# Performance work log

Hardware: AMD Instinct MI355X
Metric: run time of the kernel (lower is better)

## Reference

```python
import jax, jax.numpy as jnp
import numpy as np

B, S, D, H, F = 4, 1024, 1024, 16, 4096
DH = D // H  # 64


def _xavier(key, shape):
    fan_in, fan_out = shape[-2], shape[-1]
    limit = np.sqrt(6.0 / (fan_in + fan_out)).astype(np.float32)
    return jax.random.uniform(key, shape, jnp.float32, -limit, limit)


def setup_inputs() -> dict:
    key = jax.random.key(0)
    ks = jax.random.split(key, 24)
    inp = {
        'decoder_input': jax.random.normal(ks[0], (B, S, D), jnp.float32),
        'encoder_output': jax.random.normal(ks[1], (B, S, D), jnp.float32),
        'mask': jnp.broadcast_to(jnp.tril(jnp.ones((S, S), jnp.bool_)), (B, S, S)),
    }
    # self-attention per-head Q/K/V weights stacked over heads: (H, D, DH)
    for i, p in enumerate(['sa', 'ca']):
        base = 2 + i * 8
        inp[f'{p}_wq'] = _xavier(ks[base + 0], (H, D, DH))
        inp[f'{p}_wk'] = _xavier(ks[base + 1], (H, D, DH))
        inp[f'{p}_wv'] = _xavier(ks[base + 2], (H, D, DH))
        inp[f'{p}_bq'] = jnp.zeros((H, DH), jnp.float32)
        inp[f'{p}_bk'] = jnp.zeros((H, DH), jnp.float32)
        inp[f'{p}_bv'] = jnp.zeros((H, DH), jnp.float32)
        inp[f'{p}_wo'] = _xavier(ks[base + 3], (H * DH, D))
        inp[f'{p}_bo'] = jnp.zeros((D,), jnp.float32)
    inp['ff_w1'] = _xavier(ks[18], (D, F))
    inp['ff_b1'] = jnp.zeros((F,), jnp.float32)
    inp['ff_w2'] = _xavier(ks[19], (F, D))
    inp['ff_b2'] = jnp.zeros((D,), jnp.float32)
    for j in (1, 2, 3):
        inp[f'ln{j}_g'] = jnp.ones((D,), jnp.float32)
        inp[f'ln{j}_b'] = jnp.zeros((D,), jnp.float32)
    return inp


def _layernorm(x, g, b, eps=1e-12):
    # torch x.var() default is unbiased (ddof=1) -- match it
    mean = jnp.mean(x, axis=-1, keepdims=True)
    var = jnp.var(x, axis=-1, keepdims=True, ddof=1)
    return g * (x - mean) * jax.lax.rsqrt(var + eps) + b


def _mha(q_in, k_in, v_in, wq, bq, wk, bk, wv, bv, wo, bo, mask=None):
    scale = np.float32(1.0 / np.sqrt(DH))
    q = jnp.einsum('bsd,hde->bhse', q_in, wq) + bq[None, :, None, :]
    k = jnp.einsum('bsd,hde->bhse', k_in, wk) + bk[None, :, None, :]
    v = jnp.einsum('bsd,hde->bhse', v_in, wv) + bv[None, :, None, :]
    scores = jnp.einsum('bhqe,bhke->bhqk', q, k) * scale
    if mask is not None:
        scores = jnp.where(mask[:, None, :, :], scores, jnp.float32(-1e9))
    attn = jax.nn.softmax(scores, axis=-1)
    out = jnp.einsum('bhqk,bhke->bhqe', attn, v)  # (B,H,S,DH)
    out = out.transpose(0, 2, 1, 3).reshape(q_in.shape[0], q_in.shape[1], H * DH)
    return out @ wo + bo


def reference(decoder_input, encoder_output, mask,
              sa_wq, sa_wk, sa_wv, sa_bq, sa_bk, sa_bv, sa_wo, sa_bo,
              ca_wq, ca_wk, ca_wv, ca_bq, ca_bk, ca_bv, ca_wo, ca_bo,
              ff_w1, ff_b1, ff_w2, ff_b2,
              ln1_g, ln1_b, ln2_g, ln2_b, ln3_g, ln3_b):
    # dropout is identity (eval mode)
    out1 = _mha(decoder_input, decoder_input, decoder_input,
                sa_wq, sa_bq, sa_wk, sa_bk, sa_wv, sa_bv, sa_wo, sa_bo, mask)
    out1 = _layernorm(out1 + decoder_input, ln1_g, ln1_b)
    out2 = _mha(out1, encoder_output, encoder_output,
                ca_wq, ca_bq, ca_wk, ca_bk, ca_wv, ca_bv, ca_wo, ca_bo, None)
    out2 = _layernorm(out2 + out1, ln2_g, ln2_b)
    out3 = jax.nn.relu(out2 @ ff_w1 + ff_b1) @ ff_w2 + ff_b2
    out3 = _layernorm(out3 + out2, ln3_g, ln3_b)
    return out3
```

## Files before the change

kernel.cpp:

```cpp
#include <hip/hip_runtime.h>
#include <hip/hip_bf16.h>

using bf16 = __hip_bfloat16;
typedef __attribute__((ext_vector_type(8))) short bf16x8;
typedef __attribute__((ext_vector_type(4))) float f32x4;

__device__ __forceinline__ float toF(float x) { return x; }
__device__ __forceinline__ float toF(bf16 x) { return __bfloat162float(x); }

template <typename T> __device__ __forceinline__ T fromF(float x);
template <> __device__ __forceinline__ float fromF<float>(float x) { return x; }
template <> __device__ __forceinline__ bf16 fromF<bf16>(float x) { return __float2bfloat16(x); }

__device__ __forceinline__ unsigned short f2bu(float f) {
    bf16 h = __float2bfloat16(f);
    return *reinterpret_cast<unsigned short*>(&h);
}
__device__ __forceinline__ float bu2f(unsigned short u) {
    unsigned int x = ((unsigned int)u) << 16;
    return __uint_as_float(x);
}

__device__ __forceinline__ void gload16(const unsigned short* g, unsigned short* l) {
    __builtin_amdgcn_global_load_lds(
        (const __attribute__((address_space(1))) unsigned int*)g,
        (__attribute__((address_space(3))) unsigned int*)l, 16, 0, 0);
}

__global__ __launch_bounds__(256) void cvt_k(const float* __restrict__ X,
                                             unsigned short* __restrict__ Y, int n)
{
    int i = (blockIdx.x * 256 + threadIdx.x) * 4;
    if (i >= n) return;
    float4 v = *(const float4*)(X + i);
    ushort4 o;
    o.x = f2bu(v.x); o.y = f2bu(v.y); o.z = f2bu(v.z); o.w = f2bu(v.w);
    *(ushort4*)(Y + i) = o;
}

struct WPtrs { const float* w[3]; };

template <bool HEADED>
__global__ __launch_bounds__(256) void wtrans_k(
    WPtrs wp, unsigned short* __restrict__ Wt, int K, int N)
{
    __shared__ float t[32][33];
    const float* __restrict__ W = wp.w[blockIdx.z];
    unsigned short* __restrict__ out = Wt + (size_t)blockIdx.z * K * N;
    const int k0 = blockIdx.x * 32, n0 = blockIdx.y * 32;
    const int tx = threadIdx.x & 31, ty = threadIdx.x >> 5;
#pragma unroll
    for (int i = 0; i < 4; i++) {
        int k = k0 + ty + 8 * i, n = n0 + tx;
        float v;
        if constexpr (HEADED) v = W[((size_t)(n >> 6) * K + k) * 64 + (n & 63)];
        else                  v = W[(size_t)k * N + n];
        t[ty + 8 * i][tx] = v;
    }
    __syncthreads();
#pragma unroll
    for (int i = 0; i < 4; i++)
        out[(size_t)(n0 + ty + 8 * i) * K + k0 + tx] = f2bu(t[tx][ty + 8 * i]);
}

template <typename TO, typename TR, bool RELU, bool HASRES, int BN>
__global__ __launch_bounds__(256) void gemm_mfma(
    const unsigned short* __restrict__ A, const unsigned short* __restrict__ Bt,
    const float* __restrict__ bias, const TR* __restrict__ res,
    TO* __restrict__ C, int M, int N, int K)
{
    constexpr int MI = (BN == 128) ? 4 : 2;
    __shared__ __align__(16) unsigned short As[128 * 64];
    __shared__ __align__(16) unsigned short Bs[BN * 64];

    const int tid = threadIdx.x;
    const int lane = tid & 63, wv = tid >> 6;
    const int quad = lane >> 4, col = lane & 15;
    const int m0 = blockIdx.y * 128, n0 = blockIdx.x * BN;
    const int wm = (BN == 128) ? (wv >> 1) * 64 : wv * 32;
    const int wn = (BN == 128) ? (wv & 1) * 64 : 0;

    f32x4 acc[MI][4];
#pragma unroll
    for (int i = 0; i < MI; i++)
#pragma unroll
        for (int j = 0; j < 4; j++) acc[i][j] = (f32x4){0.f, 0.f, 0.f, 0.f};

    const int rowl = (wv << 3) + (lane >> 3);
    const int xq = (lane & 7) ^ (lane >> 3);
    const unsigned short* Ag = A + (size_t)(m0 + rowl) * K + xq * 8;
    const unsigned short* Bg = Bt + (size_t)(n0 + rowl) * K + xq * 8;
    unsigned short* AsW = As + wv * 512;
    unsigned short* BsW = Bs + wv * 512;

    const int xr = col & 7;

    for (int k0 = 0; k0 < K; k0 += 64) {
        __syncthreads();
#pragma unroll
        for (int r = 0; r < 4; r++)
            gload16(Ag + (size_t)(r * 32) * K + k0, AsW + r * 2048);
#pragma unroll
        for (int r = 0; r < BN / 32; r++)
            gload16(Bg + (size_t)(r * 32) * K + k0, BsW + r * 2048);
        __syncthreads();

#pragma unroll
        for (int kk = 0; kk < 2; kk++) {
            const int cq = ((kk << 2) + quad) ^ xr;
            bf16x8 af[MI], bfr[4];
#pragma unroll
            for (int mi = 0; mi < MI; mi++)
                af[mi] = *(const bf16x8*)(As + (wm + mi * 16 + col) * 64 + cq * 8);
#pragma unroll
            for (int ni = 0; ni < 4; ni++)
                bfr[ni] = *(const bf16x8*)(Bs + (wn + ni * 16 + col) * 64 + cq * 8);
#pragma unroll
            for (int mi = 0; mi < MI; mi++)
#pragma unroll
                for (int ni = 0; ni < 4; ni++)
                    acc[mi][ni] = __builtin_amdgcn_mfma_f32_16x16x32_bf16(
                        af[mi], bfr[ni], acc[mi][ni], 0, 0, 0);
        }
    }

    float bv[4];
#pragma unroll
    for (int ni = 0; ni < 4; ni++) bv[ni] = bias[n0 + wn + ni * 16 + col];
#pragma unroll
    for (int mi = 0; mi < MI; mi++) {
#pragma unroll
        for (int r = 0; r < 4; r++) {
            int m = m0 + wm + mi * 16 + quad * 4 + r;
#pragma unroll
            for (int ni = 0; ni < 4; ni++) {
                int n = n0 + wn + ni * 16 + col;
                float v = acc[mi][ni][r] + bv[ni];
                if constexpr (HASRES) v += toF(res[(size_t)m * N + n]);
                if constexpr (RELU) v = v > 0.f ? v : 0.f;
                C[(size_t)m * N + n] = fromF<TO>(v);
            }
        }
    }
}

struct SegArgs {
    const float* bias[3];
    unsigned short* out[3];
};

__global__ __launch_bounds__(256) void gemm_seg(
    const unsigned short* __restrict__ A, const unsigned short* __restrict__ Bt,
    SegArgs sp, int M, int K, int transSeg)
{
    __shared__ __align__(16) unsigned short As[128 * 64];
    __shared__ __align__(16) unsigned short Bs[128 * 64];

    const int tid = threadIdx.x;
    const int lane = tid & 63, wv = tid >> 6;
    const int quad = lane >> 4, col = lane & 15;
    const int m0 = blockIdx.y * 128, n0 = blockIdx.x * 128;
    const int wm = (wv >> 1) * 64, wn = (wv & 1) * 64;

    f32x4 acc[4][4];
#pragma unroll
    for (int i = 0; i < 4; i++)
#pragma unroll
        for (int j = 0; j < 4; j++) acc[i][j] = (f32x4){0.f, 0.f, 0.f, 0.f};

    const int rowl = (wv << 3) + (lane >> 3);
    const int xq = (lane & 7) ^ (lane >> 3);
    const unsigned short* Ag = A + (size_t)(m0 + rowl) * K + xq * 8;
    const unsigned short* Bg = Bt + (size_t)(n0 + rowl) * K + xq * 8;
    unsigned short* AsW = As + wv * 512;
    unsigned short* BsW = Bs + wv * 512;
    const int xr = col & 7;

    for (int k0 = 0; k0 < K; k0 += 64) {
        __syncthreads();
#pragma unroll
        for (int r = 0; r < 4; r++)
            gload16(Ag + (size_t)(r * 32) * K + k0, AsW + r * 2048);
#pragma unroll
        for (int r = 0; r < 4; r++)
            gload16(Bg + (size_t)(r * 32) * K + k0, BsW + r * 2048);
        __syncthreads();

#pragma unroll
        for (int kk = 0; kk < 2; kk++) {
            const int cq = ((kk << 2) + quad) ^ xr;
            bf16x8 af[4], bfr[4];
#pragma unroll
            for (int mi = 0; mi < 4; mi++)
                af[mi] = *(const bf16x8*)(As + (wm + mi * 16 + col) * 64 + cq * 8);
#pragma unroll
            for (int ni = 0; ni < 4; ni++)
                bfr[ni] = *(const bf16x8*)(Bs + (wn + ni * 16 + col) * 64 + cq * 8);
#pragma unroll
            for (int mi = 0; mi < 4; mi++)
#pragma unroll
                for (int ni = 0; ni < 4; ni++)
                    acc[mi][ni] = __builtin_amdgcn_mfma_f32_16x16x32_bf16(
                        af[mi], bfr[ni], acc[mi][ni], 0, 0, 0);
        }
    }

    const int seg = n0 >> 10;
    const float* bias = sp.bias[seg];
    unsigned short* out = sp.out[seg];
    const int nb = (n0 & 1023) + wn;
    const bool trans = (seg == transSeg);

    float bv[4];
#pragma unroll
    for (int ni = 0; ni < 4; ni++) bv[ni] = bias[nb + ni * 16 + col];
#pragma unroll
    for (int mi = 0; mi < 4; mi++) {
#pragma unroll
        for (int r = 0; r < 4; r++) {
            int m = m0 + wm + mi * 16 + quad * 4 + r;
#pragma unroll
            for (int ni = 0; ni < 4; ni++) {
                int nl = nb + ni * 16 + col;
                float v = acc[mi][ni][r] + bv[ni];
                if (trans)
                    out[((size_t)(m >> 10) * 1024 + nl) * 1024 + (m & 1023)] = f2bu(v);
                else
                    out[(size_t)m * 1024 + nl] = f2bu(v);
            }
        }
    }
}

template <bool CAUSAL>
__global__ __launch_bounds__(256) void fattn_k(
    const unsigned short* __restrict__ Q, const unsigned short* __restrict__ K,
    const unsigned short* __restrict__ Vt, unsigned short* __restrict__ O, int S)
{
    const int qt = CAUSAL ? ((int)gridDim.x - 1 - (int)blockIdx.x) : blockIdx.x;
    const int h = blockIdx.y, b = blockIdx.z;
    const int H64 = 1024;
    const int tid = threadIdx.x;
    const int w = tid >> 6, lane = tid & 63;
    const int quad = lane >> 4, col = lane & 15;

    __shared__ __align__(16) unsigned short Ks[64 * 72];
    __shared__ __align__(16) unsigned short Vs[64 * 72];
    __shared__ __align__(16) unsigned short Ps[4 * 16 * 72];

    const int qBase = qt * 64 + w * 16;
    const size_t qrow = ((size_t)b * S + qBase + col) * H64 + h * 64;

    const float qscale = 0.125f * 1.44269504f;
    bf16x8 qf0, qf1;
    {
        bf16x8 r0 = *(const bf16x8*)(Q + qrow + quad * 8);
        bf16x8 r1 = *(const bf16x8*)(Q + qrow + quad * 8 + 32);
#pragma unroll
        for (int j = 0; j < 8; j++) {
            qf0[j] = (short)f2bu(bu2f((unsigned short)r0[j]) * qscale);
            qf1[j] = (short)f2bu(bu2f((unsigned short)r1[j]) * qscale);
        }
    }

    f32x4 o[4];
#pragma unroll
    for (int g = 0; g < 4; g++) o[g] = (f32x4){0.f, 0.f, 0.f, 0.f};
    float m_run[4], l_run[4];
#pragma unroll
    for (int r = 0; r < 4; r++) { m_run[r] = -1e30f; l_run[r] = 0.f; }

    const int skey = tid >> 2;
    const int sseg = (tid & 3) * 16;
    const size_t kgbase = (size_t)b * S * H64 + h * 64;
    const size_t vgbase = ((size_t)b * 1024 + h * 64) * (size_t)S;

    const int nkt = CAUSAL ? (qt + 1) : (S >> 6);
    unsigned short* Pw = Ps + w * (16 * 72);

    for (int kt = 0; kt < nkt; kt++) {
        __syncthreads();
        {
            const unsigned short* kg_ = K + kgbase + (size_t)(kt * 64 + skey) * H64;
            const unsigned short* vg_ = Vt + vgbase + (size_t)skey * S + kt * 64;
            *(uint4*)(Ks + skey * 72 + sseg)     = *(const uint4*)(kg_ + sseg);
            *(uint4*)(Ks + skey * 72 + sseg + 8) = *(const uint4*)(kg_ + sseg + 8);
            *(uint4*)(Vs + skey * 72 + sseg)     = *(const uint4*)(vg_ + sseg);
            *(uint4*)(Vs + skey * 72 + sseg + 8) = *(const uint4*)(vg_ + sseg + 8);
        }
        __syncthreads();

        f32x4 s[4];
#pragma unroll
        for (int kg = 0; kg < 4; kg++) {
            bf16x8 k0 = *(const bf16x8*)(Ks + (kg * 16 + col) * 72 + quad * 8);
            bf16x8 k1 = *(const bf16x8*)(Ks + (kg * 16 + col) * 72 + quad * 8 + 32);
            f32x4 a = (f32x4){0.f, 0.f, 0.f, 0.f};
            a = __builtin_amdgcn_mfma_f32_16x16x32_bf16(qf0, k0, a, 0, 0, 0);
            a = __builtin_amdgcn_mfma_f32_16x16x32_bf16(qf1, k1, a, 0, 0, 0);
            s[kg] = a;
        }

        if (CAUSAL && kt == qt) {
#pragma unroll
            for (int kg = 0; kg < 4; kg++)
#pragma unroll
                for (int r = 0; r < 4; r++) {
                    int key = kg * 16 + col;
                    int q = w * 16 + quad * 4 + r;
                    if (key > q) s[kg][r] = -1e30f;
                }
        }

        float mx[4];
#pragma unroll
        for (int r = 0; r < 4; r++) {
            float m2 = fmaxf(fmaxf(s[0][r], s[1][r]), fmaxf(s[2][r], s[3][r]));
#pragma unroll
            for (int off = 1; off < 16; off <<= 1)
                m2 = fmaxf(m2, __shfl_xor(m2, off));
            mx[r] = m2;
        }

        bool defer = (mx[0] <= m_run[0] + 8.f) & (mx[1] <= m_run[1] + 8.f)
                   & (mx[2] <= m_run[2] + 8.f) & (mx[3] <= m_run[3] + 8.f);
        if (!__all(defer)) {
#pragma unroll
            for (int r = 0; r < 4; r++) {
                float mnew = fmaxf(m_run[r], mx[r]);
                float alpha = exp2f(m_run[r] - mnew);
                l_run[r] *= alpha;
#pragma unroll
                for (int g = 0; g < 4; g++) o[g][r] *= alpha;
                m_run[r] = mnew;
            }
        }

#pragma unroll
        for (int r = 0; r < 4; r++) {
            float ps = 0.f;
#pragma unroll
            for (int kg = 0; kg < 4; kg++) {
                float e = exp2f(s[kg][r] - m_run[r]);
                s[kg][r] = e;
                ps += e;
            }
#pragma unroll
            for (int off = 1; off < 16; off <<= 1)
                ps += __shfl_xor(ps, off);
            l_run[r] += ps;
        }

#pragma unroll
        for (int kg = 0; kg < 4; kg++)
#pragma unroll
            for (int r = 0; r < 4; r++)
                Pw[(quad * 4 + r) * 72 + kg * 16 + col] = f2bu(s[kg][r]);
        __syncthreads();

        bf16x8 p0 = *(const bf16x8*)(Pw + col * 72 + quad * 8);
        bf16x8 p1 = *(const bf16x8*)(Pw + col * 72 + quad * 8 + 32);

#pragma unroll
        for (int g = 0; g < 4; g++) {
            bf16x8 v0 = *(const bf16x8*)(Vs + (g * 16 + col) * 72 + quad * 8);
            bf16x8 v1 = *(const bf16x8*)(Vs + (g * 16 + col) * 72 + quad * 8 + 32);
            o[g] = __builtin_amdgcn_mfma_f32_16x16x32_bf16(p0, v0, o[g], 0, 0, 0);
            o[g] = __builtin_amdgcn_mfma_f32_16x16x32_bf16(p1, v1, o[g], 0, 0, 0);
        }
    }

    const size_t orow = ((size_t)b * S + qBase) * H64 + h * 64;
#pragma unroll
    for (int r = 0; r < 4; r++) {
        float inv = 1.f / l_run[r];
        int q = quad * 4 + r;
#pragma unroll
        for (int g = 0; g < 4; g++)
            O[orow + (size_t)q * H64 + g * 16 + col] = f2bu(o[g][r] * inv);
    }
}

template <typename TO>
__global__ __launch_bounds__(256) void ln_k(
    const float* __restrict__ X, const float* __restrict__ g,
    const float* __restrict__ bb, TO* __restrict__ O, int D)
{
    const int row = blockIdx.x;
    const int tid = threadIdx.x;
    __shared__ float xs[1024];
    __shared__ float red[256];
    const float* x = X + (size_t)row * D;

    float s = 0.f;
    for (int i = tid; i < D; i += 256) { float v = x[i]; xs[i] = v; s += v; }
    red[tid] = s;
    __syncthreads();
    for (int t = 128; t > 0; t >>= 1) {
        if (tid < t) red[tid] += red[tid + t];
        __syncthreads();
    }
    const float mean = red[0] / (float)D;
    __syncthreads();

    float s2 = 0.f;
    for (int i = tid; i < D; i += 256) { float d = xs[i] - mean; s2 += d * d; }
    red[tid] = s2;
    __syncthreads();
    for (int t = 128; t > 0; t >>= 1) {
        if (tid < t) red[tid] += red[tid + t];
        __syncthreads();
    }
    const float rstd = rsqrtf(red[0] / (float)(D - 1) + 1e-12f);

    TO* o = O + (size_t)row * D;
    for (int i = tid; i < D; i += 256)
        o[i] = fromF<TO>(g[i] * (xs[i] - mean) * rstd + bb[i]);
}

extern "C" void kernel_launch(void* const* d_in, const int* in_sizes, int n_in,
                              void* d_out, int out_size, void* d_ws, size_t ws_size,
                              hipStream_t stream)
{
    const int Bb = 4, S = 1024, D = 1024, F = 4096;
    const int M = Bb * S;
    const int H = 16;

    const float* dec = (const float*)d_in[0];
    const float* enc = (const float*)d_in[1];

    int base = 2;
    if (n_in >= 29 && in_sizes[2] == Bb * S * S) base = 3;

    const float* sa_wq = (const float*)d_in[base + 0];
    const float* sa_wk = (const float*)d_in[base + 1];
    const float* sa_wv = (const float*)d_in[base + 2];
    const float* sa_bq = (const float*)d_in[base + 3];
    const float* sa_bk = (const float*)d_in[base + 4];
    const float* sa_bv = (const float*)d_in[base + 5];
    const float* sa_wo = (const float*)d_in[base + 6];
    const float* sa_bo = (const float*)d_in[base + 7];
    const float* ca_wq = (const float*)d_in[base + 8];
    const float* ca_wk = (const float*)d_in[base + 9];
    const float* ca_wv = (const float*)d_in[base + 10];
    const float* ca_bq = (const float*)d_in[base + 11];
    const float* ca_bk = (const float*)d_in[base + 12];
    const float* ca_bv = (const float*)d_in[base + 13];
    const float* ca_wo = (const float*)d_in[base + 14];
    const float* ca_bo = (const float*)d_in[base + 15];
    const float* ff_w1 = (const float*)d_in[base + 16];
    const float* ff_b1 = (const float*)d_in[base + 17];
    const float* ff_w2 = (const float*)d_in[base + 18];
    const float* ff_b2 = (const float*)d_in[base + 19];
    const float* ln1_g = (const float*)d_in[base + 20];
    const float* ln1_b = (const float*)d_in[base + 21];
    const float* ln2_g = (const float*)d_in[base + 22];
    const float* ln2_b = (const float*)d_in[base + 23];
    const float* ln3_g = (const float*)d_in[base + 24];
    const float* ln3_b = (const float*)d_in[base + 25];

    const size_t E = (size_t)M * D;
    const size_t M1 = (size_t)1024 * 1024;
    float* SUM = (float*)d_ws;
    bf16* O1 = (bf16*)(SUM + E);
    bf16* O2 = O1 + E;
    bf16* Q  = O2 + E;
    bf16* Kb = Q + E;
    bf16* Vt = Kb + E;
    bf16* AO = Vt + E;
    bf16* HID = Q;
    unsigned short* decB = (unsigned short*)AO;
    unsigned short* Wt   = (unsigned short*)d_out;
    unsigned short* encB = (unsigned short*)d_out + 4 * 1024 * 1024;

    dim3 blk(256);
    dim3 gQKV(3 * D / 128, M / 128);
    dim3 gKV(2 * D / 128, M / 128);
    dim3 gN(D / 64, M / 128);
    dim3 gF(F / 128, M / 128);
    dim3 gA(S / 64, H, Bb);
    dim3 gT3(D / 32, D / 32, 3);
    dim3 gT2z(D / 32, D / 32, 2);
    dim3 gT(D / 32, D / 32, 1);
    dim3 gT1(D / 32, F / 32, 1);
    dim3 gT2(F / 32, D / 32, 1);

    cvt_k<<<M * D / 1024, blk, 0, stream>>>(dec, decB, M * D);
    cvt_k<<<M * D / 1024, blk, 0, stream>>>(enc, encB, M * D);

    {
        WPtrs wp; wp.w[0] = sa_wq; wp.w[1] = sa_wk; wp.w[2] = sa_wv;
        wtrans_k<true><<<gT3, blk, 0, stream>>>(wp, Wt, D, D);
    }
    {
        SegArgs sp;
        sp.bias[0] = sa_bq; sp.bias[1] = sa_bk; sp.bias[2] = sa_bv;
        sp.out[0] = (unsigned short*)Q; sp.out[1] = (unsigned short*)Kb;
        sp.out[2] = (unsigned short*)Vt;
        gemm_seg<<<gQKV, blk, 0, stream>>>(decB, Wt, sp, M, D, 2);
    }
    fattn_k<true><<<gA, blk, 0, stream>>>((const unsigned short*)Q, (const unsigned short*)Kb,
                                          (const unsigned short*)Vt, (unsigned short*)AO, S);
    {
        WPtrs wp; wp.w[0] = sa_wo; wp.w[1] = nullptr; wp.w[2] = nullptr;
        wtrans_k<false><<<gT, blk, 0, stream>>>(wp, Wt, D, D);
    }
    gemm_mfma<float, float, false, true, 64><<<gN, blk, 0, stream>>>(
        (const unsigned short*)AO, Wt, sa_bo, dec, SUM, M, D, D);
    ln_k<bf16><<<M, blk, 0, stream>>>(SUM, ln1_g, ln1_b, O1, D);

    {
        WPtrs wp; wp.w[0] = ca_wq; wp.w[1] = nullptr; wp.w[2] = nullptr;
        wtrans_k<true><<<gT, blk, 0, stream>>>(wp, Wt, D, D);
    }
    gemm_mfma<bf16, float, false, false, 64><<<gN, blk, 0, stream>>>(
        (const unsigned short*)O1, Wt, ca_bq, (const float*)nullptr, Q, M, D, D);
    {
        WPtrs wp; wp.w[0] = ca_wk; wp.w[1] = ca_wv; wp.w[2] = nullptr;
        wtrans_k<true><<<gT2z, blk, 0, stream>>>(wp, Wt, D, D);
    }
    {
        SegArgs sp;
        sp.bias[0] = ca_bk; sp.bias[1] = ca_bv; sp.bias[2] = nullptr;
        sp.out[0] = (unsigned short*)Kb; sp.out[1] = (unsigned short*)Vt;
        sp.out[2] = nullptr;
        gemm_seg<<<gKV, blk, 0, stream>>>(encB, Wt, sp, M, D, 1);
    }
    fattn_k<false><<<gA, blk, 0, stream>>>((const unsigned short*)Q, (const unsigned short*)Kb,
                                           (const unsigned short*)Vt, (unsigned short*)AO, S);
    {
        WPtrs wp; wp.w[0] = ca_wo; wp.w[1] = nullptr; wp.w[2] = nullptr;
        wtrans_k<false><<<gT, blk, 0, stream>>>(wp, Wt, D, D);
    }
    gemm_mfma<float, bf16, false, true, 64><<<gN, blk, 0, stream>>>(
        (const unsigned short*)AO, Wt, ca_bo, O1, SUM, M, D, D);
    ln_k<bf16><<<M, blk, 0, stream>>>(SUM, ln2_g, ln2_b, O2, D);

    {
        WPtrs wp; wp.w[0] = ff_w1; wp.w[1] = nullptr; wp.w[2] = nullptr;
        wtrans_k<false><<<gT1, blk, 0, stream>>>(wp, Wt, D, F);
    }
    gemm_mfma<bf16, float, true, false, 128><<<gF, blk, 0, stream>>>(
        (const unsigned short*)O2, Wt, ff_b1, (const float*)nullptr, HID, M, F, D);
    {
        WPtrs wp; wp.w[0] = ff_w2; wp.w[1] = nullptr; wp.w[2] = nullptr;
        wtrans_k<false><<<gT2, blk, 0, stream>>>(wp, Wt, F, D);
    }
    gemm_mfma<float, bf16, false, true, 64><<<gN, blk, 0, stream>>>(
        (const unsigned short*)HID, Wt, ff_b2, O2, SUM, M, D, F);
    ln_k<float><<<M, blk, 0, stream>>>(SUM, ln3_g, ln3_b, (float*)d_out, D);
}
```

Before: 600.8 us.

## Load K/V fragments directly from global in flash attention, use fast exp2

The flash-attention kernel no longer stages K and V tiles through shared memory. Each wave now reads its MFMA operand fragments straight from global memory, which removes the per-tile shared-memory copy and all block-wide barriers, including the one after the per-wave P write. The exp2f calls become the hardware exp2 builtin. In exchange, the four waves of a block each fetch the same K/V data, relying on caches, and global-load latency is exposed with no software prefetch. The P store and reload now rely on in-order LDS access within a wave rather than an explicit barrier.

```diff
diff --git a/kernel.cpp b/kernel.cpp
--- a/kernel.cpp
+++ b/kernel.cpp
@@ -19,6 +19,14 @@
 __device__ __forceinline__ float bu2f(unsigned short u) {
     unsigned int x = ((unsigned int)u) << 16;
     return __uint_as_float(x);
+}
+
+__device__ __forceinline__ float fexp2(float x) {
+#if __has_builtin(__builtin_amdgcn_exp2f)
+    return __builtin_amdgcn_exp2f(x);
+#else
+    return __expf(x * 0.69314718f);
+#endif
 }
 
 __device__ __forceinline__ void gload16(const unsigned short* g, unsigned short* l) {
@@ -244,8 +252,6 @@
     const int w = tid >> 6, lane = tid & 63;
     const int quad = lane >> 4, col = lane & 15;
 
-    __shared__ __align__(16) unsigned short Ks[64 * 72];
-    __shared__ __align__(16) unsigned short Vs[64 * 72];
     __shared__ __align__(16) unsigned short Ps[4 * 16 * 72];
 
     const int qBase = qt * 64 + w * 16;
@@ -270,8 +276,6 @@
 #pragma unroll
     for (int r = 0; r < 4; r++) { m_run[r] = -1e30f; l_run[r] = 0.f; }
 
-    const int skey = tid >> 2;
-    const int sseg = (tid & 3) * 16;
     const size_t kgbase = (size_t)b * S * H64 + h * 64;
     const size_t vgbase = ((size_t)b * 1024 + h * 64) * (size_t)S;
 
@@ -279,22 +283,13 @@
     unsigned short* Pw = Ps + w * (16 * 72);
 
     for (int kt = 0; kt < nkt; kt++) {
-        __syncthreads();
-        {
-            const unsigned short* kg_ = K + kgbase + (size_t)(kt * 64 + skey) * H64;
-            const unsigned short* vg_ = Vt + vgbase + (size_t)skey * S + kt * 64;
-            *(uint4*)(Ks + skey * 72 + sseg)     = *(const uint4*)(kg_ + sseg);
-            *(uint4*)(Ks + skey * 72 + sseg + 8) = *(const uint4*)(kg_ + sseg + 8);
-            *(uint4*)(Vs + skey * 72 + sseg)     = *(const uint4*)(vg_ + sseg);
-            *(uint4*)(Vs + skey * 72 + sseg + 8) = *(const uint4*)(vg_ + sseg + 8);
-        }
-        __syncthreads();
-
         f32x4 s[4];
 #pragma unroll
         for (int kg = 0; kg < 4; kg++) {
-            bf16x8 k0 = *(const bf16x8*)(Ks + (kg * 16 + col) * 72 + quad * 8);
-            bf16x8 k1 = *(const bf16x8*)(Ks + (kg * 16 + col) * 72 + quad * 8 + 32);
+            const unsigned short* kr =
+                K + kgbase + (size_t)(kt * 64 + kg * 16 + col) * H64 + quad * 8;
+            bf16x8 k0 = *(const bf16x8*)(kr);
+            bf16x8 k1 = *(const bf16x8*)(kr + 32);
             f32x4 a = (f32x4){0.f, 0.f, 0.f, 0.f};
             a = __builtin_amdgcn_mfma_f32_16x16x32_bf16(qf0, k0, a, 0, 0, 0);
             a = __builtin_amdgcn_mfma_f32_16x16x32_bf16(qf1, k1, a, 0, 0, 0);
@@ -328,7 +323,7 @@
 #pragma unroll
             for (int r = 0; r < 4; r++) {
                 float mnew = fmaxf(m_run[r], mx[r]);
-                float alpha = exp2f(m_run[r] - mnew);
+                float alpha = fexp2(m_run[r] - mnew);
                 l_run[r] *= alpha;
 #pragma unroll
                 for (int g = 0; g < 4; g++) o[g][r] *= alpha;
@@ -341,7 +336,7 @@
             float ps = 0.f;
 #pragma unroll
             for (int kg = 0; kg < 4; kg++) {
-                float e = exp2f(s[kg][r] - m_run[r]);
+                float e = fexp2(s[kg][r] - m_run[r]);
                 s[kg][r] = e;
                 ps += e;
             }
@@ -356,15 +351,16 @@
 #pragma unroll
             for (int r = 0; r < 4; r++)
                 Pw[(quad * 4 + r) * 72 + kg * 16 + col] = f2bu(s[kg][r]);
-        __syncthreads();
 
         bf16x8 p0 = *(const bf16x8*)(Pw + col * 72 + quad * 8);
         bf16x8 p1 = *(const bf16x8*)(Pw + col * 72 + quad * 8 + 32);
 
 #pragma unroll
         for (int g = 0; g < 4; g++) {
-            bf16x8 v0 = *(const bf16x8*)(Vs + (g * 16 + col) * 72 + quad * 8);
-            bf16x8 v1 = *(const bf16x8*)(Vs + (g * 16 + col) * 72 + quad * 8 + 32);
+            const unsigned short* vr =
+                Vt + vgbase + (size_t)(g * 16 + col) * S + kt * 64 + quad * 8;
+            bf16x8 v0 = *(const bf16x8*)(vr);
+            bf16x8 v1 = *(const bf16x8*)(vr + 32);
             o[g] = __builtin_amdgcn_mfma_f32_16x16x32_bf16(p0, v0, o[g], 0, 0, 0);
             o[g] = __builtin_amdgcn_mfma_f32_16x16x32_bf16(p1, v1, o[g], 0, 0, 0);
         }
@@ -460,7 +456,6 @@
     const float* ln3_b = (const float*)d_in[base + 25];
 
     const size_t E = (size_t)M * D;
-    const size_t M1 = (size_t)1024 * 1024;
     float* SUM = (float*)d_ws;
     bf16* O1 = (bf16*)(SUM + E);
     bf16* O2 = O1 + E;
```

After: 700.0 us. 1.17x slower.
